# Kernel optimization log

Measured on AMD Instinct MI355X. Metric: run time of the kernel, lower is better.

Reference implementation:

```python
import jax, jax.numpy as jnp
import numpy as np

B, C, H, W = 8, 384, 128, 128
WSZ = 8          # window size
DH = 32          # dim per head
HEADS = C // DH  # 12
INNER = HEADS * DH
EPS = 1e-5


def setup_inputs() -> dict:
    key = jax.random.key(0)
    ks = jax.random.split(key, 6)
    x = jax.random.normal(ks[0], (B, C, H, W), jnp.float32)
    skip = jax.random.normal(ks[1], (B, C, H, W), jnp.float32)
    # LayerNorm affine params (shape (1, C, 1, 1) in torch; store as (C,))
    g_q = jnp.ones((C,), jnp.float32)
    b_q = jnp.zeros((C,), jnp.float32)
    g_kv = jnp.ones((C,), jnp.float32)
    b_kv = jnp.zeros((C,), jnp.float32)
    # 1x1 conv weights: [out_channels, in_channels]
    Wq = jax.random.normal(ks[2], (INNER, C), jnp.float32) * 0.05
    Wkv = jax.random.normal(ks[3], (2 * INNER, C), jnp.float32) * 0.05
    Wout = jax.random.normal(ks[4], (C, INNER), jnp.float32) * 0.05
    bout = jax.random.normal(ks[5], (C,), jnp.float32) * 0.05
    return dict(x=x, skip=skip, g_q=g_q, b_q=b_q, g_kv=g_kv, b_kv=b_kv,
                Wq=Wq, Wkv=Wkv, Wout=Wout, bout=bout)


def _channel_ln(x, g, b):
    # LayerNorm over channel dim (axis=1), biased variance
    mean = jnp.mean(x, axis=1, keepdims=True)
    var = jnp.mean((x - mean) ** 2, axis=1, keepdims=True)
    return (x - mean) / jnp.sqrt(var + EPS) * g[None, :, None, None] + b[None, :, None, None]


def _to_windows(x):
    # [B, C, H, W] -> [B*nh*nw, C, wsz, wsz]
    b, c, h, w = x.shape
    nh, nw = h // WSZ, w // WSZ
    x = x.reshape(b, c, nh, WSZ, nw, WSZ).transpose(0, 2, 4, 1, 3, 5)
    return x.reshape(b * nh * nw, c, WSZ, WSZ)


def _from_windows(x, b, h, w):
    # [B*nh*nw, C, wsz, wsz] -> [B, C, H, W]
    nh, nw = h // WSZ, w // WSZ
    c = x.shape[1]
    x = x.reshape(b, nh, nw, c, WSZ, WSZ).transpose(0, 3, 1, 4, 2, 5)
    return x.reshape(b, c, h, w)


def _split_heads(t):
    # [Bw, heads*dh, wsz, wsz] -> [Bw, heads, wsz*wsz, dh]
    bw = t.shape[0]
    t = t.reshape(bw, HEADS, DH, WSZ * WSZ)
    return t.transpose(0, 1, 3, 2)


def reference(x, skip, g_q, b_q, g_kv, b_kv, Wq, Wkv, Wout, bout):
    b, _, h, w = x.shape
    xn = _to_windows(_channel_ln(x, g_q, b_q))
    skn = _to_windows(_channel_ln(skip, g_kv, b_kv))
    # 1x1 convs as channel GEMMs
    q = jnp.einsum('oc,bcxy->boxy', Wq, xn)
    kv = jnp.einsum('oc,bcxy->boxy', Wkv, skn)
    k, v = kv[:, :INNER], kv[:, INNER:]
    q, k, v = _split_heads(q), _split_heads(k), _split_heads(v)
    scale = DH ** -0.5
    attn = jax.nn.softmax(jnp.einsum('bhqd,bhkd->bhqk', q, k) * scale, axis=-1)
    out = jnp.einsum('bhqk,bhkd->bhqd', attn, v)
    # [Bw, heads, S, dh] -> [Bw, inner, wsz, wsz]
    out = out.transpose(0, 1, 3, 2).reshape(-1, INNER, WSZ, WSZ)
    out = jnp.einsum('oc,bcxy->boxy', Wout, out) + bout[None, :, None, None]
    return _from_windows(out, b, h, w)
```

## Files before the change

### kernel.cpp

```cpp
#include <hip/hip_runtime.h>
#include <stdint.h>

typedef __attribute__((ext_vector_type(4))) float f32x4;
typedef __attribute__((ext_vector_type(8))) short s16x8;
typedef unsigned int u32;
typedef unsigned short u16;

#define DEVFN static __device__ __forceinline__

constexpr int C = 384;
constexpr int WIMG = 128;
constexpr int HW = 128 * 128;
constexpr float EPS = 1e-5f;
constexpr float QSCALE = 0.17677669529663687f;

constexpr int R1 = 0;
constexpr int R2 = 49152;
constexpr int R3 = 98304;
constexpr int PR = 147456;
constexpr int LDS_BYTES = 163840;

DEVFN u16 f2bf(float f) {
  union { float f; u32 u; } v; v.f = f;
  u32 r = v.u + 0x7fffu + ((v.u >> 16) & 1u);
  return (u16)(r >> 16);
}
DEVFN f32x4 MFMA(s16x8 a, s16x8 b, f32x4 c) {
  return __builtin_amdgcn_mfma_f32_16x16x32_bf16(a, b, c, 0, 0, 0);
}
DEVFN int adr768(int base, int row, int b) { return base + row * 768 + (b ^ ((row & 7) << 4)); }
DEVFN int adr128(int base, int row, int b) { return base + row * 128 + (b ^ ((row & 7) << 4)); }

__global__ void cvt_bf16_kernel(const float* __restrict__ src, u16* __restrict__ dst, int n) {
  int i = (blockIdx.x * blockDim.x + threadIdx.x) * 4;
  if (i + 3 < n) {
    f32x4 v = *(const f32x4*)(src + i);
    u32* d = (u32*)(dst + i);
    d[0] = (u32)f2bf(v[0]) | ((u32)f2bf(v[1]) << 16);
    d[1] = (u32)f2bf(v[2]) | ((u32)f2bf(v[3]) << 16);
  }
}

__global__ void fold_ln_weights(const float* __restrict__ Wq, const float* __restrict__ Wkv,
                                const float* __restrict__ gq, const float* __restrict__ bq,
                                const float* __restrict__ gkv, const float* __restrict__ bkv,
                                u16* __restrict__ wqb, u16* __restrict__ wkb, u16* __restrict__ wvb,
                                float* __restrict__ sg_all, float* __restrict__ sb_all) {
  int r = blockIdx.x * 4 + (threadIdx.x >> 6);
  int lane = threadIdx.x & 63;
  const float* src; const float* g; const float* b; u16* dst; float scale;
  if (r < 384) { src = Wq + (size_t)r * C; g = gq; b = bq; dst = wqb + (size_t)r * C; scale = QSCALE; }
  else {
    src = Wkv + (size_t)(r - 384) * C; g = gkv; b = bkv; scale = 1.f;
    dst = (r < 768) ? wkb + (size_t)(r - 384) * C : wvb + (size_t)(r - 768) * C;
  }
  float sg = 0.f, sb = 0.f;
#pragma unroll
  for (int i = 0; i < 6; ++i) {
    int c = lane + i * 64;
    float wv = src[c], gg = g[c];
    sg += wv * gg; sb += wv * b[c];
    dst[c] = f2bf(wv * gg * scale);
  }
#pragma unroll
  for (int m = 1; m < 64; m <<= 1) { sg += __shfl_xor(sg, m); sb += __shfl_xor(sb, m); }
  if (lane == 0) { sg_all[r] = sg * scale; sb_all[r] = sb * scale; }
}

__launch_bounds__(512, 2)
__global__ void fused_win_attn(
    const float* __restrict__ x, const float* __restrict__ skip,
    const u16* __restrict__ wqb, const u16* __restrict__ wkb,
    const u16* __restrict__ wvb, const u16* __restrict__ wob,
    const float* __restrict__ sg_all, const float* __restrict__ sb_all,
    const float* __restrict__ bout, float* __restrict__ out) {
  extern __shared__ char smem[];
  const int tid = threadIdx.x;
  const int lane = tid & 63;
  const int w = tid >> 6;
  const int l15 = lane & 15;
  const int lg = lane >> 4;
  const int kco = lg * 8;

  const int bid = blockIdx.x;
  const int win = (bid & 7) * 256 + (bid >> 3);
  const int bimg = win >> 8;
  const int Y0 = ((win >> 4) & 15) * 8;
  const int X0 = (win & 15) * 8;
  const size_t img_off = (size_t)bimg * C * HW;

  const f32x4 fzero = {0.f, 0.f, 0.f, 0.f};

  float* stats_x = (float*)(smem + PR);
  float* stats_s = (float*)(smem + PR + 512);
  float* red = (float*)(smem + PR + 1024);

  const int p = tid & 63;
  const int g8 = tid >> 6;
  const int yy = p >> 3, xx = p & 7;

  for (int tt = 0; tt < 2; ++tt) {
    const float* src = tt ? skip : x;
    const int RB = tt ? R2 : R1;
    const float* gb = src + img_off + (size_t)(Y0 + yy) * WIMG + X0 + xx;
    float s = 0.f, q = 0.f;
#pragma unroll
    for (int i = 0; i < 24; ++i) {
      int c0 = g8 * 48 + i * 2;
      float v0 = gb[(size_t)c0 * HW];
      float v1 = gb[(size_t)c0 * HW + HW];
      s += v0 + v1; q += v0 * v0 + v1 * v1;
      *(u32*)(smem + adr768(RB, p, c0 * 2)) = (u32)f2bf(v0) | ((u32)f2bf(v1) << 16);
    }
    red[tid * 2] = s; red[tid * 2 + 1] = q;
    __syncthreads();
    if (tid < 64) {
      float sm = 0.f, sq = 0.f;
#pragma unroll
      for (int gg = 0; gg < 8; ++gg) { sm += red[(gg * 64 + tid) * 2]; sq += red[(gg * 64 + tid) * 2 + 1]; }
      float mean = sm * (1.f / 384.f);
      float var = sq * (1.f / 384.f) - mean * mean;
      float* st = tt ? stats_s : stats_x;
      st[tid * 2] = mean; st[tid * 2 + 1] = 1.f / sqrtf(var + EPS);
    }
    __syncthreads();
  }

  {
    f32x4 acc[3][4];
#pragma unroll
    for (int nn = 0; nn < 3; ++nn)
#pragma unroll
      for (int m = 0; m < 4; ++m) acc[nn][m] = fzero;
#pragma unroll
    for (int k = 0; k < 12; ++k) {
      s16x8 A[4];
#pragma unroll
      for (int m = 0; m < 4; ++m)
        A[m] = *(const s16x8*)(smem + adr768(R2, m * 16 + l15, (k * 32 + kco) * 2));
#pragma unroll
      for (int nn = 0; nn < 3; ++nn) {
        s16x8 B = *(const s16x8*)(wkb + (size_t)((3 * w + nn) * 16 + l15) * C + k * 32 + kco);
#pragma unroll
        for (int m = 0; m < 4; ++m) acc[nn][m] = MFMA(A[m], B, acc[nn][m]);
      }
    }
    float sg3[3], sb3[3];
#pragma unroll
    for (int nn = 0; nn < 3; ++nn) {
      int o = (3 * w + nn) * 16 + l15;
      sg3[nn] = sg_all[384 + o]; sb3[nn] = sb_all[384 + o];
    }
#pragma unroll
    for (int m = 0; m < 4; ++m)
#pragma unroll
      for (int j = 0; j < 4; ++j) {
        int tok = m * 16 + lg * 4 + j;
        float mn = stats_s[tok * 2], rs = stats_s[tok * 2 + 1];
#pragma unroll
        for (int nn = 0; nn < 3; ++nn) {
          int o = (3 * w + nn) * 16 + l15;
          float val = rs * acc[nn][m][j] - rs * mn * sg3[nn] + sb3[nn];
          *(u16*)(smem + adr768(R3, tok, o * 2)) = f2bf(val);
        }
      }
  }

  {
    f32x4 acc[3][4];
#pragma unroll
    for (int mm = 0; mm < 3; ++mm)
#pragma unroll
      for (int n = 0; n < 4; ++n) acc[mm][n] = fzero;
#pragma unroll
    for (int k = 0; k < 12; ++k) {
      s16x8 Bv[4];
#pragma unroll
      for (int n = 0; n < 4; ++n)
        Bv[n] = *(const s16x8*)(smem + adr768(R2, n * 16 + l15, (k * 32 + kco) * 2));
#pragma unroll
      for (int mm = 0; mm < 3; ++mm) {
        s16x8 A = *(const s16x8*)(wvb + (size_t)((3 * w + mm) * 16 + l15) * C + k * 32 + kco);
#pragma unroll
        for (int n = 0; n < 4; ++n) acc[mm][n] = MFMA(A, Bv[n], acc[mm][n]);
      }
    }
    float mn4[4], rs4[4];
#pragma unroll
    for (int n = 0; n < 4; ++n) {
      int tok = n * 16 + l15;
      mn4[n] = stats_s[tok * 2]; rs4[n] = stats_s[tok * 2 + 1];
    }
    __syncthreads();
#pragma unroll
    for (int mm = 0; mm < 3; ++mm)
#pragma unroll
      for (int j = 0; j < 4; ++j) {
        int dh = (3 * w + mm) * 16 + lg * 4 + j;
        float sg = sg_all[768 + dh], sb = sb_all[768 + dh];
#pragma unroll
        for (int n = 0; n < 4; ++n) {
          int tok = n * 16 + l15;
          float val = rs4[n] * acc[mm][n][j] - rs4[n] * mn4[n] * sg + sb;
          *(u16*)(smem + adr128(R2, dh, tok * 2)) = f2bf(val);
        }
      }
  }

  {
    f32x4 acc[3][4];
#pragma unroll
    for (int nn = 0; nn < 3; ++nn)
#pragma unroll
      for (int m = 0; m < 4; ++m) acc[nn][m] = fzero;
#pragma unroll
    for (int k = 0; k < 12; ++k) {
      s16x8 A[4];
#pragma unroll
      for (int m = 0; m < 4; ++m)
        A[m] = *(const s16x8*)(smem + adr768(R1, m * 16 + l15, (k * 32 + kco) * 2));
#pragma unroll
      for (int nn = 0; nn < 3; ++nn) {
        s16x8 B = *(const s16x8*)(wqb + (size_t)((3 * w + nn) * 16 + l15) * C + k * 32 + kco);
#pragma unroll
        for (int m = 0; m < 4; ++m) acc[nn][m] = MFMA(A[m], B, acc[nn][m]);
      }
    }
    float sg3[3], sb3[3];
#pragma unroll
    for (int nn = 0; nn < 3; ++nn) {
      int o = (3 * w + nn) * 16 + l15;
      sg3[nn] = sg_all[o]; sb3[nn] = sb_all[o];
    }
    __syncthreads();
#pragma unroll
    for (int m = 0; m < 4; ++m)
#pragma unroll
      for (int j = 0; j < 4; ++j) {
        int tok = m * 16 + lg * 4 + j;
        float mn = stats_x[tok * 2], rs = stats_x[tok * 2 + 1];
#pragma unroll
        for (int nn = 0; nn < 3; ++nn) {
          int o = (3 * w + nn) * 16 + l15;
          float val = rs * acc[nn][m][j] - rs * mn * sg3[nn] + sb3[nn];
          *(u16*)(smem + adr768(R1, tok, o * 2)) = f2bf(val);
        }
      }
  }
  __syncthreads();

  f32x4 outacc[6][4];
#pragma unroll
  for (int nn = 0; nn < 6; ++nn)
#pragma unroll
    for (int m = 0; m < 4; ++m) outacc[nn][m] = fzero;

  const int wq = w & 3;
  const int hpar = (w >= 4) ? 1 : 0;
  char* PH = smem + PR + hpar * 8192;

  for (int t = 0; t < 6; ++t) {
    const int ha = 2 * t + hpar;
    s16x8 WB[6];
#pragma unroll
    for (int nn = 0; nn < 6; ++nn)
      WB[nn] = *(const s16x8*)(wob + (size_t)((wq * 6 + nn) * 16 + l15) * C + ha * 32 + kco);

    {
      s16x8 aq = *(const s16x8*)(smem + adr768(R1, wq * 16 + l15, (ha * 32 + kco) * 2));
      f32x4 sv[4];
#pragma unroll
      for (int n = 0; n < 4; ++n) {
        s16x8 bk = *(const s16x8*)(smem + adr768(R3, n * 16 + l15, (ha * 32 + kco) * 2));
        sv[n] = MFMA(aq, bk, fzero);
      }
#pragma unroll
      for (int j = 0; j < 4; ++j) {
        float mx = fmaxf(fmaxf(sv[0][j], sv[1][j]), fmaxf(sv[2][j], sv[3][j]));
#pragma unroll
        for (int msk = 1; msk < 16; msk <<= 1) mx = fmaxf(mx, __shfl_xor(mx, msk));
        float e0 = __expf(sv[0][j] - mx);
        float e1 = __expf(sv[1][j] - mx);
        float e2 = __expf(sv[2][j] - mx);
        float e3 = __expf(sv[3][j] - mx);
        float sum = e0 + e1 + e2 + e3;
#pragma unroll
        for (int msk = 1; msk < 16; msk <<= 1) sum += __shfl_xor(sum, msk);
        float inv = 1.0f / sum;
        int row = wq * 16 + lg * 4 + j;
        int sw = (row & 7) << 4;
        *(u16*)(PH + row * 128 + (((0 * 16 + l15) * 2) ^ sw)) = f2bf(e0 * inv);
        *(u16*)(PH + row * 128 + (((1 * 16 + l15) * 2) ^ sw)) = f2bf(e1 * inv);
        *(u16*)(PH + row * 128 + (((2 * 16 + l15) * 2) ^ sw)) = f2bf(e2 * inv);
        *(u16*)(PH + row * 128 + (((3 * 16 + l15) * 2) ^ sw)) = f2bf(e3 * inv);
      }
    }
    f32x4 ov[2] = {fzero, fzero};
#pragma unroll
    for (int ks = 0; ks < 2; ++ks) {
      int prow = wq * 16 + l15;
      s16x8 ap = *(const s16x8*)(PH + prow * 128 + (((ks * 32 + kco) * 2) ^ ((prow & 7) << 4)));
#pragma unroll
      for (int n = 0; n < 2; ++n) {
        s16x8 bv = *(const s16x8*)(smem + adr128(R2, ha * 32 + n * 16 + l15, (ks * 32 + kco) * 2));
        ov[n] = MFMA(ap, bv, ov[n]);
      }
    }
    __syncthreads();
#pragma unroll
    for (int n = 0; n < 2; ++n)
#pragma unroll
      for (int j = 0; j < 4; ++j)
        *(u16*)(PH + (wq * 16 + lg * 4 + j) * 80 + (n * 16 + l15) * 2) = f2bf(ov[n][j]);
    __syncthreads();
    {
      s16x8 ao[4];
#pragma unroll
      for (int m = 0; m < 4; ++m)
        ao[m] = *(const s16x8*)(PH + (m * 16 + l15) * 80 + kco * 2);
#pragma unroll
      for (int nn = 0; nn < 6; ++nn)
#pragma unroll
        for (int m = 0; m < 4; ++m)
          outacc[nn][m] = MFMA(ao[m], WB[nn], outacc[nn][m]);
    }
    __syncthreads();
  }

  float* outf = (float*)smem;
  if (w < 4) {
#pragma unroll
    for (int nn = 0; nn < 6; ++nn) {
      int o = (wq * 6 + nn) * 16 + l15;
      float bo = bout[o];
#pragma unroll
      for (int m = 0; m < 4; ++m)
#pragma unroll
        for (int j = 0; j < 4; ++j)
          outf[(m * 16 + lg * 4 + j) * 385 + o] = outacc[nn][m][j] + bo;
    }
  }
  __syncthreads();
  if (w >= 4) {
#pragma unroll
    for (int nn = 0; nn < 6; ++nn) {
      int o = (wq * 6 + nn) * 16 + l15;
#pragma unroll
      for (int m = 0; m < 4; ++m)
#pragma unroll
        for (int j = 0; j < 4; ++j)
          outf[(m * 16 + lg * 4 + j) * 385 + o] += outacc[nn][m][j];
    }
  }
  __syncthreads();
  {
    float* ob = out + img_off + (size_t)(Y0 + yy) * WIMG + X0 + xx;
#pragma unroll
    for (int i = 0; i < 48; ++i) {
      int c = g8 * 48 + i;
      ob[(size_t)c * HW] = outf[p * 385 + c];
    }
  }
}

extern "C" void kernel_launch(void* const* d_in, const int* in_sizes, int n_in,
                              void* d_out, int out_size, void* d_ws, size_t ws_size,
                              hipStream_t stream) {
  const float* x    = (const float*)d_in[0];
  const float* skip = (const float*)d_in[1];
  const float* gq   = (const float*)d_in[2];
  const float* bq   = (const float*)d_in[3];
  const float* gkv  = (const float*)d_in[4];
  const float* bkv  = (const float*)d_in[5];
  const float* Wq   = (const float*)d_in[6];
  const float* Wkv  = (const float*)d_in[7];
  const float* Wout = (const float*)d_in[8];
  const float* bout = (const float*)d_in[9];
  float* out = (float*)d_out;

  char* ws = (char*)d_ws;
  u16* wqb = (u16*)(ws);
  u16* wkb = (u16*)(ws + 294912);
  u16* wvb = (u16*)(ws + 589824);
  u16* wob = (u16*)(ws + 884736);
  float* sg_all = (float*)(ws + 1179648);
  float* sb_all = (float*)(ws + 1184256);

  hipFuncSetAttribute((const void*)fused_win_attn,
                      hipFuncAttributeMaxDynamicSharedMemorySize, LDS_BYTES);

  fold_ln_weights<<<288, 256, 0, stream>>>(Wq, Wkv, gq, bq, gkv, bkv, wqb, wkb, wvb, sg_all, sb_all);
  cvt_bf16_kernel<<<144, 256, 0, stream>>>(Wout, wob, 147456);

  fused_win_attn<<<2048, 512, LDS_BYTES, stream>>>(
      x, skip, wqb, wkb, wvb, wob, sg_all, sb_all, bout, out);
}
```

Measured before the change: 531.7 us.

## Restructure attention phase into per-warp head strips and separate output GEMM

Each warp now owns one 16-query tile and six heads. It computes S^T with K as the A operand, does the softmax reductions with two cross-lane shuffles, and stages P and O in a private 2KB LDS strip. This removes the three block-wide barriers per head pair in the old loop. The per-head outputs are written back into the Q buffer, and the output projection runs as one standard GEMM over all warps, which also removes the two-phase partial-sum reduction. The V and Q projections are also computed back-to-back before a single barrier, at the cost of holding more accumulator registers live.

```diff
diff --git a/kernel.cpp b/kernel.cpp
--- a/kernel.cpp
+++ b/kernel.cpp
@@ -91,9 +91,9 @@
 
   const f32x4 fzero = {0.f, 0.f, 0.f, 0.f};
 
-  float* stats_x = (float*)(smem + PR);
-  float* stats_s = (float*)(smem + PR + 512);
-  float* red = (float*)(smem + PR + 1024);
+  float* red = (float*)(smem + PR);
+  float* stats_x = (float*)(smem + PR + 4096);
+  float* stats_s = (float*)(smem + PR + 4608);
 
   const int p = tid & 63;
   const int g8 = tid >> 6;
@@ -145,33 +145,27 @@
         for (int m = 0; m < 4; ++m) acc[nn][m] = MFMA(A[m], B, acc[nn][m]);
       }
     }
-    float sg3[3], sb3[3];
 #pragma unroll
     for (int nn = 0; nn < 3; ++nn) {
       int o = (3 * w + nn) * 16 + l15;
-      sg3[nn] = sg_all[384 + o]; sb3[nn] = sb_all[384 + o];
-    }
-#pragma unroll
-    for (int m = 0; m < 4; ++m)
-#pragma unroll
-      for (int j = 0; j < 4; ++j) {
-        int tok = m * 16 + lg * 4 + j;
-        float mn = stats_s[tok * 2], rs = stats_s[tok * 2 + 1];
-#pragma unroll
-        for (int nn = 0; nn < 3; ++nn) {
-          int o = (3 * w + nn) * 16 + l15;
-          float val = rs * acc[nn][m][j] - rs * mn * sg3[nn] + sb3[nn];
-          *(u16*)(smem + adr768(R3, tok, o * 2)) = f2bf(val);
+      float sg = sg_all[384 + o], sb = sb_all[384 + o];
+#pragma unroll
+      for (int m = 0; m < 4; ++m)
+#pragma unroll
+        for (int j = 0; j < 4; ++j) {
+          int tok = m * 16 + lg * 4 + j;
+          float mn = stats_s[tok * 2], rs = stats_s[tok * 2 + 1];
+          *(u16*)(smem + adr768(R3, tok, o * 2)) = f2bf(rs * acc[nn][m][j] - rs * mn * sg + sb);
         }
-      }
-  }
-
-  {
-    f32x4 acc[3][4];
+    }
+  }
+
+  f32x4 accV[3][4];
+  {
 #pragma unroll
     for (int mm = 0; mm < 3; ++mm)
 #pragma unroll
-      for (int n = 0; n < 4; ++n) acc[mm][n] = fzero;
+      for (int n = 0; n < 4; ++n) accV[mm][n] = fzero;
 #pragma unroll
     for (int k = 0; k < 12; ++k) {
       s16x8 Bv[4];
@@ -182,16 +176,34 @@
       for (int mm = 0; mm < 3; ++mm) {
         s16x8 A = *(const s16x8*)(wvb + (size_t)((3 * w + mm) * 16 + l15) * C + k * 32 + kco);
 #pragma unroll
-        for (int n = 0; n < 4; ++n) acc[mm][n] = MFMA(A, Bv[n], acc[mm][n]);
-      }
-    }
-    float mn4[4], rs4[4];
-#pragma unroll
-    for (int n = 0; n < 4; ++n) {
-      int tok = n * 16 + l15;
-      mn4[n] = stats_s[tok * 2]; rs4[n] = stats_s[tok * 2 + 1];
-    }
-    __syncthreads();
+        for (int n = 0; n < 4; ++n) accV[mm][n] = MFMA(A, Bv[n], accV[mm][n]);
+      }
+    }
+  }
+
+  f32x4 accQ[3][4];
+  {
+#pragma unroll
+    for (int nn = 0; nn < 3; ++nn)
+#pragma unroll
+      for (int m = 0; m < 4; ++m) accQ[nn][m] = fzero;
+#pragma unroll
+    for (int k = 0; k < 12; ++k) {
+      s16x8 A[4];
+#pragma unroll
+      for (int m = 0; m < 4; ++m)
+        A[m] = *(const s16x8*)(smem + adr768(R1, m * 16 + l15, (k * 32 + kco) * 2));
+#pragma unroll
+      for (int nn = 0; nn < 3; ++nn) {
+        s16x8 B = *(const s16x8*)(wqb + (size_t)((3 * w + nn) * 16 + l15) * C + k * 32 + kco);
+#pragma unroll
+        for (int m = 0; m < 4; ++m) accQ[nn][m] = MFMA(A[m], B, accQ[nn][m]);
+      }
+    }
+  }
+  __syncthreads();
+
+  {
 #pragma unroll
     for (int mm = 0; mm < 3; ++mm)
 #pragma unroll
@@ -201,156 +213,121 @@
 #pragma unroll
         for (int n = 0; n < 4; ++n) {
           int tok = n * 16 + l15;
-          float val = rs4[n] * acc[mm][n][j] - rs4[n] * mn4[n] * sg + sb;
-          *(u16*)(smem + adr128(R2, dh, tok * 2)) = f2bf(val);
+          float mn = stats_s[tok * 2], rs = stats_s[tok * 2 + 1];
+          *(u16*)(smem + adr128(R2, dh, tok * 2)) = f2bf(rs * accV[mm][n][j] - rs * mn * sg + sb);
         }
       }
-  }
-
-  {
-    f32x4 acc[3][4];
-#pragma unroll
-    for (int nn = 0; nn < 3; ++nn)
-#pragma unroll
-      for (int m = 0; m < 4; ++m) acc[nn][m] = fzero;
-#pragma unroll
-    for (int k = 0; k < 12; ++k) {
-      s16x8 A[4];
-#pragma unroll
-      for (int m = 0; m < 4; ++m)
-        A[m] = *(const s16x8*)(smem + adr768(R1, m * 16 + l15, (k * 32 + kco) * 2));
-#pragma unroll
-      for (int nn = 0; nn < 3; ++nn) {
-        s16x8 B = *(const s16x8*)(wqb + (size_t)((3 * w + nn) * 16 + l15) * C + k * 32 + kco);
-#pragma unroll
-        for (int m = 0; m < 4; ++m) acc[nn][m] = MFMA(A[m], B, acc[nn][m]);
-      }
-    }
-    float sg3[3], sb3[3];
 #pragma unroll
     for (int nn = 0; nn < 3; ++nn) {
       int o = (3 * w + nn) * 16 + l15;
-      sg3[nn] = sg_all[o]; sb3[nn] = sb_all[o];
-    }
-    __syncthreads();
-#pragma unroll
-    for (int m = 0; m < 4; ++m)
+      float sg = sg_all[o], sb = sb_all[o];
+#pragma unroll
+      for (int m = 0; m < 4; ++m)
+#pragma unroll
+        for (int j = 0; j < 4; ++j) {
+          int tok = m * 16 + lg * 4 + j;
+          float mn = stats_x[tok * 2], rs = stats_x[tok * 2 + 1];
+          *(u16*)(smem + adr768(R1, tok, o * 2)) = f2bf(rs * accQ[nn][m][j] - rs * mn * sg + sb);
+        }
+    }
+  }
+  __syncthreads();
+
+  const int qt = w & 3;
+  const int hh = w >> 2;
+  char* strip = smem + PR + w * 2048;
+  const int swzq = (l15 & 7) << 4;
+
+  s16x8 oA[6];
+
+#pragma unroll
+  for (int hloc = 0; hloc < 6; ++hloc) {
+    const int h = hh * 6 + hloc;
+    s16x8 bq = *(const s16x8*)(smem + adr768(R1, qt * 16 + l15, h * 64 + lg * 16));
+    f32x4 sc[4];
+#pragma unroll
+    for (int m = 0; m < 4; ++m) {
+      s16x8 ak = *(const s16x8*)(smem + adr768(R3, m * 16 + l15, h * 64 + lg * 16));
+      sc[m] = MFMA(ak, bq, fzero);
+    }
+    float mx = sc[0][0];
+#pragma unroll
+    for (int m = 0; m < 4; ++m)
+#pragma unroll
+      for (int j = 0; j < 4; ++j) mx = fmaxf(mx, sc[m][j]);
+    mx = fmaxf(mx, __shfl_xor(mx, 16));
+    mx = fmaxf(mx, __shfl_xor(mx, 32));
+    float ex[4][4];
+    float sum = 0.f;
+#pragma unroll
+    for (int m = 0; m < 4; ++m)
+#pragma unroll
+      for (int j = 0; j < 4; ++j) { float e = __expf(sc[m][j] - mx); ex[m][j] = e; sum += e; }
+    sum += __shfl_xor(sum, 16);
+    sum += __shfl_xor(sum, 32);
+    float inv = 1.0f / sum;
+#pragma unroll
+    for (int m = 0; m < 4; ++m)
+#pragma unroll
+      for (int j2 = 0; j2 < 2; ++j2) {
+        u32 pk = (u32)f2bf(ex[m][2 * j2] * inv) | ((u32)f2bf(ex[m][2 * j2 + 1] * inv) << 16);
+        *(u32*)(strip + l15 * 128 + ((m * 32 + lg * 8 + j2 * 4) ^ swzq)) = pk;
+      }
+    f32x4 ov[2] = {fzero, fzero};
+#pragma unroll
+    for (int ks = 0; ks < 2; ++ks) {
+      s16x8 ap = *(const s16x8*)(strip + l15 * 128 + ((ks * 64 + lg * 16) ^ swzq));
+#pragma unroll
+      for (int n = 0; n < 2; ++n) {
+        s16x8 bv = *(const s16x8*)(smem + adr128(R2, h * 32 + n * 16 + l15, ks * 64 + lg * 16));
+        ov[n] = MFMA(ap, bv, ov[n]);
+      }
+    }
+#pragma unroll
+    for (int n = 0; n < 2; ++n)
 #pragma unroll
       for (int j = 0; j < 4; ++j) {
-        int tok = m * 16 + lg * 4 + j;
-        float mn = stats_x[tok * 2], rs = stats_x[tok * 2 + 1];
-#pragma unroll
-        for (int nn = 0; nn < 3; ++nn) {
-          int o = (3 * w + nn) * 16 + l15;
-          float val = rs * acc[nn][m][j] - rs * mn * sg3[nn] + sb3[nn];
-          *(u16*)(smem + adr768(R1, tok, o * 2)) = f2bf(val);
-        }
-      }
-  }
-  __syncthreads();
-
-  f32x4 outacc[6][4];
-#pragma unroll
-  for (int nn = 0; nn < 6; ++nn)
+        int row = lg * 4 + j;
+        *(u16*)(strip + row * 128 + ((n * 32 + l15 * 2) ^ ((row & 7) << 4))) = f2bf(ov[n][j]);
+      }
+    oA[hloc] = *(const s16x8*)(strip + l15 * 128 + ((lg * 16) ^ swzq));
+  }
+
+#pragma unroll
+  for (int hloc = 0; hloc < 6; ++hloc)
+    *(s16x8*)(smem + adr768(R1, qt * 16 + l15, (hh * 6 + hloc) * 64 + lg * 16)) = oA[hloc];
+  __syncthreads();
+
+  f32x4 outacc[3][4];
+#pragma unroll
+  for (int nn = 0; nn < 3; ++nn)
 #pragma unroll
     for (int m = 0; m < 4; ++m) outacc[nn][m] = fzero;
-
-  const int wq = w & 3;
-  const int hpar = (w >= 4) ? 1 : 0;
-  char* PH = smem + PR + hpar * 8192;
-
-  for (int t = 0; t < 6; ++t) {
-    const int ha = 2 * t + hpar;
-    s16x8 WB[6];
-#pragma unroll
-    for (int nn = 0; nn < 6; ++nn)
-      WB[nn] = *(const s16x8*)(wob + (size_t)((wq * 6 + nn) * 16 + l15) * C + ha * 32 + kco);
-
-    {
-      s16x8 aq = *(const s16x8*)(smem + adr768(R1, wq * 16 + l15, (ha * 32 + kco) * 2));
-      f32x4 sv[4];
-#pragma unroll
-      for (int n = 0; n < 4; ++n) {
-        s16x8 bk = *(const s16x8*)(smem + adr768(R3, n * 16 + l15, (ha * 32 + kco) * 2));
-        sv[n] = MFMA(aq, bk, fzero);
-      }
-#pragma unroll
-      for (int j = 0; j < 4; ++j) {
-        float mx = fmaxf(fmaxf(sv[0][j], sv[1][j]), fmaxf(sv[2][j], sv[3][j]));
-#pragma unroll
-        for (int msk = 1; msk < 16; msk <<= 1) mx = fmaxf(mx, __shfl_xor(mx, msk));
-        float e0 = __expf(sv[0][j] - mx);
-        float e1 = __expf(sv[1][j] - mx);
-        float e2 = __expf(sv[2][j] - mx);
-        float e3 = __expf(sv[3][j] - mx);
-        float sum = e0 + e1 + e2 + e3;
-#pragma unroll
-        for (int msk = 1; msk < 16; msk <<= 1) sum += __shfl_xor(sum, msk);
-        float inv = 1.0f / sum;
-        int row = wq * 16 + lg * 4 + j;
-        int sw = (row & 7) << 4;
-        *(u16*)(PH + row * 128 + (((0 * 16 + l15) * 2) ^ sw)) = f2bf(e0 * inv);
-        *(u16*)(PH + row * 128 + (((1 * 16 + l15) * 2) ^ sw)) = f2bf(e1 * inv);
-        *(u16*)(PH + row * 128 + (((2 * 16 + l15) * 2) ^ sw)) = f2bf(e2 * inv);
-        *(u16*)(PH + row * 128 + (((3 * 16 + l15) * 2) ^ sw)) = f2bf(e3 * inv);
-      }
-    }
-    f32x4 ov[2] = {fzero, fzero};
-#pragma unroll
-    for (int ks = 0; ks < 2; ++ks) {
-      int prow = wq * 16 + l15;
-      s16x8 ap = *(const s16x8*)(PH + prow * 128 + (((ks * 32 + kco) * 2) ^ ((prow & 7) << 4)));
-#pragma unroll
-      for (int n = 0; n < 2; ++n) {
-        s16x8 bv = *(const s16x8*)(smem + adr128(R2, ha * 32 + n * 16 + l15, (ks * 32 + kco) * 2));
-        ov[n] = MFMA(ap, bv, ov[n]);
-      }
-    }
-    __syncthreads();
-#pragma unroll
-    for (int n = 0; n < 2; ++n)
+#pragma unroll
+  for (int k = 0; k < 12; ++k) {
+    s16x8 A[4];
+#pragma unroll
+    for (int m = 0; m < 4; ++m)
+      A[m] = *(const s16x8*)(smem + adr768(R1, m * 16 + l15, (k * 32 + kco) * 2));
+#pragma unroll
+    for (int nn = 0; nn < 3; ++nn) {
+      s16x8 B = *(const s16x8*)(wob + (size_t)((3 * w + nn) * 16 + l15) * C + k * 32 + kco);
+#pragma unroll
+      for (int m = 0; m < 4; ++m) outacc[nn][m] = MFMA(A[m], B, outacc[nn][m]);
+    }
+  }
+  __syncthreads();
+
+  float* outf = (float*)smem;
+#pragma unroll
+  for (int nn = 0; nn < 3; ++nn) {
+    int o = (3 * w + nn) * 16 + l15;
+    float bo = bout[o];
+#pragma unroll
+    for (int m = 0; m < 4; ++m)
 #pragma unroll
       for (int j = 0; j < 4; ++j)
-        *(u16*)(PH + (wq * 16 + lg * 4 + j) * 80 + (n * 16 + l15) * 2) = f2bf(ov[n][j]);
-    __syncthreads();
-    {
-      s16x8 ao[4];
-#pragma unroll
-      for (int m = 0; m < 4; ++m)
-        ao[m] = *(const s16x8*)(PH + (m * 16 + l15) * 80 + kco * 2);
-#pragma unroll
-      for (int nn = 0; nn < 6; ++nn)
-#pragma unroll
-        for (int m = 0; m < 4; ++m)
-          outacc[nn][m] = MFMA(ao[m], WB[nn], outacc[nn][m]);
-    }
-    __syncthreads();
-  }
-
-  float* outf = (float*)smem;
-  if (w < 4) {
-#pragma unroll
-    for (int nn = 0; nn < 6; ++nn) {
-      int o = (wq * 6 + nn) * 16 + l15;
-      float bo = bout[o];
-#pragma unroll
-      for (int m = 0; m < 4; ++m)
-#pragma unroll
-        for (int j = 0; j < 4; ++j)
-          outf[(m * 16 + lg * 4 + j) * 385 + o] = outacc[nn][m][j] + bo;
-    }
-  }
-  __syncthreads();
-  if (w >= 4) {
-#pragma unroll
-    for (int nn = 0; nn < 6; ++nn) {
-      int o = (wq * 6 + nn) * 16 + l15;
-#pragma unroll
-      for (int m = 0; m < 4; ++m)
-#pragma unroll
-        for (int j = 0; j < 4; ++j)
-          outf[(m * 16 + lg * 4 + j) * 385 + o] += outacc[nn][m][j];
-    }
+        outf[(m * 16 + lg * 4 + j) * 385 + o] = outacc[nn][m][j] + bo;
   }
   __syncthreads();
   {
```

New measurement: 599.1 us. 1.13x slower.
